# Kernel tuning notes

Measured on AMD Instinct MI355X. Metric: run time of the kernel, lower is better.

## Reference

```python
import jax, jax.numpy as jnp
import numpy as np

H = 16  # num_heads

def setup_inputs() -> dict:
    key = jax.random.key(0)
    ks = jax.random.split(key, 5)
    B, L, D = 2, 2048, 1024
    x = jax.random.normal(ks[0], (B, L, D), dtype=jnp.float32)
    # causal mask: masked_fill where mask == 0
    attn_mask = jnp.tril(jnp.ones((L, L), dtype=jnp.int32))
    scale = 1.0 / np.sqrt(D)
    Wq = jax.random.normal(ks[1], (D, D), dtype=jnp.float32) * scale
    Wk = jax.random.normal(ks[2], (D, D), dtype=jnp.float32) * scale
    Wv = jax.random.normal(ks[3], (D, D), dtype=jnp.float32) * scale
    Wo = jax.random.normal(ks[4], (D, D), dtype=jnp.float32) * scale
    return {"x": x, "attn_mask": attn_mask, "Wq": Wq, "Wk": Wk, "Wv": Wv, "Wo": Wo}

def reference(x, attn_mask, Wq, Wk, Wv, Wo):
    B, L, D = x.shape
    dh = D // H
    # nn.Linear with no bias: y = x @ W^T
    q = (x @ Wq.T).reshape(B, L, H, dh)
    k = (x @ Wk.T).reshape(B, L, H, dh)
    v = (x @ Wv.T).reshape(B, L, H, dh)
    # scores: [B, H, L, L]
    scores = jnp.einsum('blhd,bmhd->bhlm', q, k) / jnp.sqrt(jnp.array(dh, x.dtype))
    scores = jnp.where(attn_mask == 0, -jnp.inf, scores)
    attn = jax.nn.softmax(scores, axis=-1)
    out = jnp.einsum('bhlm,bmhd->blhd', attn, v).reshape(B, L, D)
    return out @ Wo.T
```

## Files before the change

### kernel.cpp

```cpp
#include <hip/hip_runtime.h>
#include <math.h>

#define L_SEQ  2048
#define D_MODEL 1024
#define N_HEAD 16
#define D_HEAD 64
#define B_SIZE 2

typedef __attribute__((ext_vector_type(8))) short bf16x8;
typedef __attribute__((ext_vector_type(4))) float f32x4;
typedef unsigned short u16;
typedef unsigned int u32;

__device__ __forceinline__ f32x4 mfma16(bf16x8 a, bf16x8 b, f32x4 c) {
    return __builtin_amdgcn_mfma_f32_16x16x32_bf16(a, b, c, 0, 0, 0);
}

__device__ __forceinline__ u16 f2bf(float x) {
    u32 u = __builtin_bit_cast(u32, x);
    u32 r = (u + 0x7FFFu + ((u >> 16) & 1u)) >> 16;
    return (u16)r;
}
__device__ __forceinline__ float bf2f(u16 h) {
    u32 u = ((u32)h) << 16;
    return __builtin_bit_cast(float, u);
}

__device__ __forceinline__ void gl2lds16(const void* g, void* l) {
    __builtin_amdgcn_global_load_lds(
        (__attribute__((address_space(1))) void*)(g),
        (__attribute__((address_space(3))) void*)(l), 16, 0, 0);
}

__global__ __launch_bounds__(256) void split_hl(const float* __restrict__ in,
                                                u16* __restrict__ out) {
    const int idx = blockIdx.x * 256 + threadIdx.x;
    const int c4 = idx << 2;
    const int r = c4 >> 10, c = c4 & 1023;
    float4 v = *(const float4*)(in + c4);
    u16 h0 = f2bf(v.x), h1 = f2bf(v.y), h2 = f2bf(v.z), h3 = f2bf(v.w);
    ushort4 hi = make_ushort4(h0, h1, h2, h3);
    ushort4 lo = make_ushort4(f2bf(v.x - bf2f(h0)), f2bf(v.y - bf2f(h1)),
                              f2bf(v.z - bf2f(h2)), f2bf(v.w - bf2f(h3)));
    *(ushort4*)(out + (size_t)r * 2048 + c) = hi;
    *(ushort4*)(out + (size_t)r * 2048 + 1024 + c) = lo;
}

__global__ __launch_bounds__(256) void split_w4(
    const float* __restrict__ w0, const float* __restrict__ w1,
    const float* __restrict__ w2, const float* __restrict__ w3,
    u16* __restrict__ outbase) {
    const float* in = (blockIdx.y == 0) ? w0 : (blockIdx.y == 1) ? w1
                      : (blockIdx.y == 2) ? w2 : w3;
    u16* out = outbase + (size_t)blockIdx.y * 2097152;
    const int idx = blockIdx.x * 256 + threadIdx.x;
    const int c4 = idx << 2;
    const int r = c4 >> 10, c = c4 & 1023;
    float4 v = *(const float4*)(in + c4);
    u16 h0 = f2bf(v.x), h1 = f2bf(v.y), h2 = f2bf(v.z), h3 = f2bf(v.w);
    ushort4 hi = make_ushort4(h0, h1, h2, h3);
    ushort4 lo = make_ushort4(f2bf(v.x - bf2f(h0)), f2bf(v.y - bf2f(h1)),
                              f2bf(v.z - bf2f(h2)), f2bf(v.w - bf2f(h3)));
    *(ushort4*)(out + (size_t)r * 2048 + c) = hi;
    *(ushort4*)(out + (size_t)r * 2048 + 1024 + c) = lo;
}

template <int MODE>
__global__ __launch_bounds__(256) void gemm_ks(
    const u16* __restrict__ A2, const u16* __restrict__ Wbase,
    float* __restrict__ Cout,
    u16* __restrict__ Qh, u16* __restrict__ Ql,
    u16* __restrict__ Kh, u16* __restrict__ Kl,
    u16* __restrict__ Vh, u16* __restrict__ Vl) {
    __shared__ __align__(16) u16 As[128 * 32];
    __shared__ __align__(16) u16 Ws[128 * 32];
    const int t = threadIdx.x, l = t & 63, wid = t >> 6;
    const int m0 = blockIdx.y << 7, n0 = blockIdx.x << 7;
    const int z = (MODE == 1) ? blockIdx.z : 0;
    const u16* W2 = Wbase + (size_t)z * (1024 * 2048);

    f32x4 acc[4][4];
#pragma unroll
    for (int i = 0; i < 4; ++i)
#pragma unroll
        for (int j = 0; j < 4; ++j) acc[i][j] = (f32x4){0.f, 0.f, 0.f, 0.f};

    int orow[2], ocs[2];
#pragma unroll
    for (int p = 0; p < 2; ++p) {
        int o = wid * 1024 + l * 16 + p * 4096;
        orow[p] = o >> 6;
        ocs[p] = ((o >> 4) & 3) ^ ((o >> 6) & 3);
    }
    const int wr = (wid >> 1) << 6, wc = (wid & 1) << 6;

    for (int k0 = 0; k0 < 3072; k0 += 32) {
        const int rg3 = k0 >> 10, kb = k0 & 1023;
        const int ka = (rg3 == 1 ? 1024 : 0) + kb;
        const int kw = (rg3 == 0 ? 1024 : 0) + kb;
        __syncthreads();
#pragma unroll
        for (int p = 0; p < 2; ++p) {
            gl2lds16(A2 + (size_t)(m0 + orow[p]) * 2048 + ka + ocs[p] * 8,
                     (u16*)As + (wid * 512 + p * 2048));
            gl2lds16(W2 + (size_t)(n0 + orow[p]) * 2048 + kw + ocs[p] * 8,
                     (u16*)Ws + (wid * 512 + p * 2048));
        }
        __syncthreads();
        bf16x8 af[4], bfr[4];
#pragma unroll
        for (int f = 0; f < 4; ++f) {
            int row = wr + (f << 4) + (l & 15);
            int ch = (l >> 4) ^ (row & 3);
            af[f] = *(const bf16x8*)&As[(row << 5) + (ch << 3)];
            int rown = wc + (f << 4) + (l & 15);
            int chn = (l >> 4) ^ (rown & 3);
            bfr[f] = *(const bf16x8*)&Ws[(rown << 5) + (chn << 3)];
        }
#pragma unroll
        for (int fm = 0; fm < 4; ++fm)
#pragma unroll
            for (int fn = 0; fn < 4; ++fn)
                acc[fm][fn] = mfma16(af[fm], bfr[fn], acc[fm][fn]);
    }

#pragma unroll
    for (int fm = 0; fm < 4; ++fm)
#pragma unroll
        for (int fn = 0; fn < 4; ++fn)
#pragma unroll
            for (int rg = 0; rg < 4; ++rg) {
                int gm = m0 + wr + (fm << 4) + ((l >> 4) << 2) + rg;
                int gn = n0 + wc + (fn << 4) + (l & 15);
                float v = acc[fm][fn][rg];
                if (MODE == 0) {
                    Cout[(size_t)gm * 1024 + gn] = v;
                } else {
                    if (z == 0) v *= 0.125f;
                    int b = gm >> 11, lq = gm & 2047, h = gn >> 6, d = gn & 63;
                    size_t oi = (((size_t)(b * 16 + h)) * 2048 + lq) * 64 + d;
                    u16 hi = f2bf(v);
                    u16 lo = f2bf(v - bf2f(hi));
                    u16 *ph, *pl;
                    if (z == 0)      { ph = Qh; pl = Ql; }
                    else if (z == 1) { ph = Kh; pl = Kl; }
                    else             { ph = Vh; pl = Vl; }
                    ph[oi] = hi;
                    pl[oi] = lo;
                }
            }
}

__global__ __launch_bounds__(128) void vtrans(const u16* __restrict__ Vh,
                                              const u16* __restrict__ Vl,
                                              u16* __restrict__ Vth,
                                              u16* __restrict__ Vtl) {
    const int t = threadIdx.x;
    const int kt = blockIdx.x, h = blockIdx.y, b = blockIdx.z;
    const size_t base = ((size_t)(b * 16 + h)) * 131072;
    const int kv0 = kt << 6;
    const u16* src = (t < 64) ? Vh : Vl;
    u16* dst = (t < 64) ? Vth : Vtl;
    const int st = t & 63;
    const int r0 = (st >> 3) << 3;
    const int c0 = (st & 7) << 3;
    ushort4 inv[8][2];
#pragma unroll
    for (int j = 0; j < 8; ++j) {
        const u16* p = src + base + (size_t)(kv0 + r0 + j) * 64 + c0;
        inv[j][0] = *(const ushort4*)p;
        inv[j][1] = *(const ushort4*)(p + 4);
    }
#pragma unroll
    for (int i = 0; i < 8; ++i) {
        u16 o[8];
#pragma unroll
        for (int j = 0; j < 8; ++j) {
            ushort4 vv = inv[j][i >> 2];
            const int ii = i & 3;
            o[j] = (ii == 0) ? vv.x : (ii == 1) ? vv.y : (ii == 2) ? vv.z : vv.w;
        }
        u16* q = dst + base + (size_t)(c0 + i) * 2048 + kv0 + r0;
        *(ushort4*)q = make_ushort4(o[0], o[1], o[2], o[3]);
        *(ushort4*)(q + 4) = make_ushort4(o[4], o[5], o[6], o[7]);
    }
}

struct QTileState {
    bf16x8 qhf[2], qlf[2];
    f32x4 oacc[4];
    float mrow[4], lrow[4];
};

__device__ __forceinline__ void qstate_init(
    QTileState& st, const u16* Qh, const u16* Ql, size_t hb, int q0, int w, int l) {
    const int rowq = q0 + (w << 4) + (l & 15);
#pragma unroll
    for (int kc = 0; kc < 2; ++kc) {
        const size_t off = hb + (size_t)rowq * 64 + (((kc << 2) + (l >> 4)) << 3);
        st.qhf[kc] = *(const bf16x8*)(Qh + off);
        st.qlf[kc] = *(const bf16x8*)(Ql + off);
    }
#pragma unroll
    for (int i = 0; i < 4; ++i) {
        st.oacc[i] = (f32x4){0.f, 0.f, 0.f, 0.f};
        st.mrow[i] = -INFINITY;
        st.lrow[i] = 0.f;
    }
}

__device__ __forceinline__ void fa_compute(
    QTileState& st, const u16* bKh, const u16* bKl,
    const u16* bVh, const u16* bVl, int kv0, int q0, int w, int l, u16* Pw) {
    if (kv0 > q0 + (w << 4) + 15) return;

    f32x4 sacc[4];
#pragma unroll
    for (int nf = 0; nf < 4; ++nf) sacc[nf] = (f32x4){0.f, 0.f, 0.f, 0.f};
#pragma unroll
    for (int kc = 0; kc < 2; ++kc) {
        bf16x8 kh_[4], kl_[4];
#pragma unroll
        for (int nf = 0; nf < 4; ++nf) {
            const int row = (nf << 4) + (l & 15);
            const int ch = ((kc << 2) + (l >> 4)) ^ (row & 7);
            kh_[nf] = *(const bf16x8*)&bKh[(row << 6) + (ch << 3)];
            kl_[nf] = *(const bf16x8*)&bKl[(row << 6) + (ch << 3)];
        }
#pragma unroll
        for (int nf = 0; nf < 4; ++nf) {
            sacc[nf] = mfma16(st.qhf[kc], kl_[nf], sacc[nf]);
            sacc[nf] = mfma16(st.qlf[kc], kh_[nf], sacc[nf]);
            sacc[nf] = mfma16(st.qhf[kc], kh_[nf], sacc[nf]);
        }
    }

    const bool domask = (kv0 + 63) > (q0 + (w << 4));
    float pm[4] = {-INFINITY, -INFINITY, -INFINITY, -INFINITY};
    float sv[4][4];
#pragma unroll
    for (int nf = 0; nf < 4; ++nf)
#pragma unroll
        for (int rg = 0; rg < 4; ++rg) {
            float x = sacc[nf][rg];
            if (domask) {
                const int colg = kv0 + (nf << 4) + (l & 15);
                const int rowg = q0 + (w << 4) + ((l >> 4) << 2) + rg;
                if (colg > rowg) x = -INFINITY;
            }
            sv[nf][rg] = x;
            pm[rg] = fmaxf(pm[rg], x);
        }
#pragma unroll
    for (int rg = 0; rg < 4; ++rg) {
        float v = pm[rg];
        v = fmaxf(v, __shfl_xor(v, 1));
        v = fmaxf(v, __shfl_xor(v, 2));
        v = fmaxf(v, __shfl_xor(v, 4));
        v = fmaxf(v, __shfl_xor(v, 8));
        pm[rg] = v;
    }
    float al[4];
#pragma unroll
    for (int rg = 0; rg < 4; ++rg) {
        const float mn = fmaxf(st.mrow[rg], pm[rg]);
        al[rg] = __expf(st.mrow[rg] - mn);
        st.mrow[rg] = mn;
    }
    float ps[4] = {0.f, 0.f, 0.f, 0.f};
    u16 pb[4][4];
#pragma unroll
    for (int nf = 0; nf < 4; ++nf)
#pragma unroll
        for (int rg = 0; rg < 4; ++rg) {
            const float p = __expf(sv[nf][rg] - st.mrow[rg]);
            ps[rg] += p;
            pb[nf][rg] = f2bf(p);
        }
#pragma unroll
    for (int rg = 0; rg < 4; ++rg) {
        float v = ps[rg];
        v += __shfl_xor(v, 1);
        v += __shfl_xor(v, 2);
        v += __shfl_xor(v, 4);
        v += __shfl_xor(v, 8);
        st.lrow[rg] = st.lrow[rg] * al[rg] + v;
    }
#pragma unroll
    for (int nf = 0; nf < 4; ++nf)
#pragma unroll
        for (int rg = 0; rg < 4; ++rg) st.oacc[nf][rg] *= al[rg];

#pragma unroll
    for (int nf = 0; nf < 4; ++nf)
#pragma unroll
        for (int rg = 0; rg < 4; ++rg) {
            const int r = ((l >> 4) << 2) + rg;
            const int c = (nf << 4) + (l & 15);
            const int ch = (c >> 3) ^ (r & 7);
            Pw[(r << 6) + (ch << 3) + (c & 7)] = pb[nf][rg];
        }
#pragma unroll
    for (int kc = 0; kc < 2; ++kc) {
        const int r = l & 15;
        const int chp = ((kc << 2) + (l >> 4)) ^ (r & 7);
        const bf16x8 pa = *(const bf16x8*)&Pw[(r << 6) + (chp << 3)];
        bf16x8 vh_[4], vl_[4];
#pragma unroll
        for (int nf = 0; nf < 4; ++nf) {
            const int row = (nf << 4) + (l & 15);
            const int cv = ((kc << 2) + (l >> 4)) ^ (row & 7);
            vh_[nf] = *(const bf16x8*)&bVh[(row << 6) + (cv << 3)];
            vl_[nf] = *(const bf16x8*)&bVl[(row << 6) + (cv << 3)];
        }
#pragma unroll
        for (int nf = 0; nf < 4; ++nf) {
            st.oacc[nf] = mfma16(pa, vh_[nf], st.oacc[nf]);
            st.oacc[nf] = mfma16(pa, vl_[nf], st.oacc[nf]);
        }
    }
}

__device__ __forceinline__ void fa_epilogue(
    QTileState& st, u16* A2, int g, int q0, int w, int l) {
    const int b = g >> 4, h = g & 15;
    float inv[4];
#pragma unroll
    for (int rg = 0; rg < 4; ++rg) inv[rg] = 1.0f / st.lrow[rg];
#pragma unroll
    for (int nf = 0; nf < 4; ++nf)
#pragma unroll
        for (int rg = 0; rg < 4; ++rg) {
            const int rowq = q0 + (w << 4) + ((l >> 4) << 2) + rg;
            const int m = (b << 11) + rowq;
            const int d = (nf << 4) + (l & 15);
            const float v = st.oacc[nf][rg] * inv[rg];
            const u16 hi = f2bf(v);
            const u16 lo = f2bf(v - bf2f(hi));
            const size_t rb = (size_t)m * 2048;
            A2[rb + h * 64 + d] = hi;
            A2[rb + 1024 + h * 64 + d] = lo;
        }
}

__global__ __launch_bounds__(512) void flash_mfma(
    const u16* __restrict__ Qh, const u16* __restrict__ Ql,
    const u16* __restrict__ Kh, const u16* __restrict__ Kl,
    const u16* __restrict__ Vth, const u16* __restrict__ Vtl,
    u16* __restrict__ A2) {
    extern __shared__ __align__(16) u16 smem[];
    u16* const KhsA = smem;
    u16* const KlsA = smem + 4096;
    u16* const VhsA = smem + 8192;
    u16* const VlsA = smem + 12288;
    u16* const KhsB = smem + 16384;
    u16* const KlsB = smem + 20480;
    u16* const VhsB = smem + 24576;
    u16* const VlsB = smem + 28672;
    u16* const Ps   = smem + 32768;

    const int t = threadIdx.x, l = t & 63, w = t >> 6;
    const int id = blockIdx.x;
    const int nid = ((id & 7) << 5) + (id >> 3);
    const int g = nid >> 3;
    const int p = nid & 7;
    const int q0A = p << 7;
    const int q0B = (15 - p) << 7;
    const size_t hb = (size_t)g * 131072;

    QTileState stA, stB;
    qstate_init(stA, Qh, Ql, hb, q0A, w, l);
    qstate_init(stB, Qh, Ql, hb, q0B, w, l);

    const int row_s = t >> 3;
    const int cs_s = (t & 7) ^ (row_s & 7);

    auto stage = [&](u16* dKh, u16* dKl, u16* dVh, u16* dVl, int kt_) {
        const int kv0s = kt_ << 6;
        const size_t koff = hb + (size_t)(kv0s + row_s) * 64 + cs_s * 8;
        gl2lds16(Kh + koff, dKh + t * 8);
        gl2lds16(Kl + koff, dKl + t * 8);
        const size_t voff = hb + (size_t)row_s * 2048 + kv0s + cs_s * 8;
        gl2lds16(Vth + voff, dVh + t * 8);
        gl2lds16(Vtl + voff, dVl + t * 8);
    };

    u16* const Pw = Ps + (w << 10);
    const int ntA = (p << 1) + 2;
    const int ntB = 32 - (p << 1);

    stage(KhsA, KlsA, VhsA, VlsA, 0);
    __syncthreads();
    for (int kt = 0; kt < ntB; kt += 2) {
        stage(KhsB, KlsB, VhsB, VlsB, kt + 1);
        fa_compute(stB, KhsA, KlsA, VhsA, VlsA, kt << 6, q0B, w, l, Pw);
        if (kt < ntA)
            fa_compute(stA, KhsA, KlsA, VhsA, VlsA, kt << 6, q0A, w, l, Pw);
        __syncthreads();
        if (kt + 2 < ntB) stage(KhsA, KlsA, VhsA, VlsA, kt + 2);
        fa_compute(stB, KhsB, KlsB, VhsB, VlsB, (kt + 1) << 6, q0B, w, l, Pw);
        if (kt + 1 < ntA)
            fa_compute(stA, KhsB, KlsB, VhsB, VlsB, (kt + 1) << 6, q0A, w, l, Pw);
        __syncthreads();
    }

    fa_epilogue(stA, A2, g, q0A, w, l);
    fa_epilogue(stB, A2, g, q0B, w, l);
}

__global__ __launch_bounds__(256) void gemm_bt_f32(
    const float* __restrict__ A, const float* __restrict__ W,
    float* __restrict__ C, int M, int N, int K) {
    __shared__ float As[16][68];
    __shared__ float Bs[16][68];
    const int t = threadIdx.x;
    const int tx = t & 15, ty = t >> 4;
    const int m0 = blockIdx.y << 6, n0 = blockIdx.x << 6;
    const int lr = t >> 2, lc = (t & 3) << 2;
    const float* Ag = A + (size_t)(m0 + lr) * K + lc;
    const float* Wg = W + (size_t)(n0 + lr) * K + lc;
    float acc[4][4];
#pragma unroll
    for (int i = 0; i < 4; ++i)
#pragma unroll
        for (int j = 0; j < 4; ++j) acc[i][j] = 0.f;
    for (int k0 = 0; k0 < K; k0 += 16) {
        const float4 av = *(const float4*)(Ag + k0);
        const float4 wv = *(const float4*)(Wg + k0);
        __syncthreads();
        As[lc + 0][lr] = av.x; As[lc + 1][lr] = av.y;
        As[lc + 2][lr] = av.z; As[lc + 3][lr] = av.w;
        Bs[lc + 0][lr] = wv.x; Bs[lc + 1][lr] = wv.y;
        Bs[lc + 2][lr] = wv.z; Bs[lc + 3][lr] = wv.w;
        __syncthreads();
#pragma unroll
        for (int kk = 0; kk < 16; ++kk) {
            const float4 a = *(const float4*)&As[kk][ty << 2];
            const float4 b = *(const float4*)&Bs[kk][tx << 2];
            acc[0][0] += a.x * b.x; acc[0][1] += a.x * b.y; acc[0][2] += a.x * b.z; acc[0][3] += a.x * b.w;
            acc[1][0] += a.y * b.x; acc[1][1] += a.y * b.y; acc[1][2] += a.y * b.z; acc[1][3] += a.y * b.w;
            acc[2][0] += a.z * b.x; acc[2][1] += a.z * b.y; acc[2][2] += a.z * b.z; acc[2][3] += a.z * b.w;
            acc[3][0] += a.w * b.x; acc[3][1] += a.w * b.y; acc[3][2] += a.w * b.z; acc[3][3] += a.w * b.w;
        }
    }
#pragma unroll
    for (int i = 0; i < 4; ++i) {
        float4 o;
        o.x = acc[i][0]; o.y = acc[i][1]; o.z = acc[i][2]; o.w = acc[i][3];
        *(float4*)&C[(size_t)(m0 + (ty << 2) + i) * N + n0 + (tx << 2)] = o;
    }
}

#define SW(row, seg) ((((seg) ^ (((row) + ((row) >> 4)) & 15)) << 2))

__global__ __launch_bounds__(256) void flash_f32(
    const float* __restrict__ Q, const float* __restrict__ K,
    const float* __restrict__ V, float* __restrict__ O) {
    __shared__ float Qs[64 * 64];
    __shared__ float KPs[64 * 64];
    __shared__ float Vs[64 * 64];
    const int t = threadIdx.x;
    const int tx = t & 15, ty = t >> 4;
    const int qt = blockIdx.x, h = blockIdx.y, b = blockIdx.z;
    const int q0 = qt << 6;
    const size_t hbase = (size_t)b * L_SEQ * D_MODEL + (size_t)h * D_HEAD;
#pragma unroll
    for (int i = 0; i < 4; ++i) {
        const int idx = t + (i << 8);
        const int rr = idx >> 4, seg = idx & 15;
        const float4 qv = *(const float4*)&Q[hbase + (size_t)(q0 + rr) * D_MODEL + (seg << 2)];
        *(float4*)&Qs[rr * 64 + SW(rr, seg)] = qv;
    }
    float m[4], lr_[4], oacc[4][4];
#pragma unroll
    for (int i = 0; i < 4; ++i) {
        m[i] = -INFINITY; lr_[i] = 0.f;
#pragma unroll
        for (int j = 0; j < 4; ++j) oacc[i][j] = 0.f;
    }
    const int ntile = qt + 1;
    for (int kt = 0; kt < ntile; ++kt) {
        const int kv0 = kt << 6;
        __syncthreads();
#pragma unroll
        for (int i = 0; i < 4; ++i) {
            const int idx = t + (i << 8);
            const int rr = idx >> 4, seg = idx & 15;
            const float4 kv = *(const float4*)&K[hbase + (size_t)(kv0 + rr) * D_MODEL + (seg << 2)];
            const float4 vv = *(const float4*)&V[hbase + (size_t)(kv0 + rr) * D_MODEL + (seg << 2)];
            *(float4*)&KPs[rr * 64 + SW(rr, seg)] = kv;
            *(float4*)&Vs[rr * 64 + SW(rr, seg)] = vv;
        }
        __syncthreads();
        float s[4][4];
#pragma unroll
        for (int i = 0; i < 4; ++i)
#pragma unroll
            for (int j = 0; j < 4; ++j) s[i][j] = 0.f;
#pragma unroll
        for (int seg = 0; seg < 16; ++seg) {
            float4 qv[4], kv[4];
#pragma unroll
            for (int i = 0; i < 4; ++i) {
                const int R = (ty << 2) + i;
                qv[i] = *(const float4*)&Qs[R * 64 + SW(R, seg)];
            }
#pragma unroll
            for (int j = 0; j < 4; ++j) {
                const int Cc = (tx << 2) + j;
                kv[j] = *(const float4*)&KPs[Cc * 64 + SW(Cc, seg)];
            }
#pragma unroll
            for (int i = 0; i < 4; ++i)
#pragma unroll
                for (int j = 0; j < 4; ++j)
                    s[i][j] += qv[i].x * kv[j].x + qv[i].y * kv[j].y +
                               qv[i].z * kv[j].z + qv[i].w * kv[j].w;
        }
        const bool diag = (kt == qt);
        float tm[4];
#pragma unroll
        for (int i = 0; i < 4; ++i) {
            tm[i] = -INFINITY;
#pragma unroll
            for (int j = 0; j < 4; ++j) {
                float sval = s[i][j] * 0.125f;
                if (diag) {
                    const int Cg = kv0 + (tx << 2) + j;
                    const int Rg = q0 + (ty << 2) + i;
                    if (Cg > Rg) sval = -INFINITY;
                }
                s[i][j] = sval;
                tm[i] = fmaxf(tm[i], sval);
            }
            tm[i] = fmaxf(tm[i], __shfl_xor(tm[i], 1));
            tm[i] = fmaxf(tm[i], __shfl_xor(tm[i], 2));
            tm[i] = fmaxf(tm[i], __shfl_xor(tm[i], 4));
            tm[i] = fmaxf(tm[i], __shfl_xor(tm[i], 8));
        }
        float p[4][4];
#pragma unroll
        for (int i = 0; i < 4; ++i) {
            const float mn = fmaxf(m[i], tm[i]);
            const float alpha = __expf(m[i] - mn);
            m[i] = mn;
            float psum = 0.f;
#pragma unroll
            for (int j = 0; j < 4; ++j) {
                p[i][j] = __expf(s[i][j] - mn);
                psum += p[i][j];
            }
            psum += __shfl_xor(psum, 1);
            psum += __shfl_xor(psum, 2);
            psum += __shfl_xor(psum, 4);
            psum += __shfl_xor(psum, 8);
            lr_[i] = lr_[i] * alpha + psum;
#pragma unroll
            for (int j = 0; j < 4; ++j) oacc[i][j] *= alpha;
        }
        __syncthreads();
#pragma unroll
        for (int i = 0; i < 4; ++i) {
            const int R = (ty << 2) + i;
            float4 pv;
            pv.x = p[i][0]; pv.y = p[i][1]; pv.z = p[i][2]; pv.w = p[i][3];
            *(float4*)&KPs[R * 64 + SW(R, tx)] = pv;
        }
        __syncthreads();
#pragma unroll
        for (int cs = 0; cs < 16; ++cs) {
            float pc[4][4];
            float4 vr[4];
#pragma unroll
            for (int i = 0; i < 4; ++i) {
                const int R = (ty << 2) + i;
                const float4 pr = *(const float4*)&KPs[R * 64 + SW(R, cs)];
                pc[i][0] = pr.x; pc[i][1] = pr.y; pc[i][2] = pr.z; pc[i][3] = pr.w;
            }
#pragma unroll
            for (int cc = 0; cc < 4; ++cc) {
                const int Cr = (cs << 2) + cc;
                vr[cc] = *(const float4*)&Vs[Cr * 64 + SW(Cr, tx)];
            }
#pragma unroll
            for (int i = 0; i < 4; ++i)
#pragma unroll
                for (int cc = 0; cc < 4; ++cc) {
                    oacc[i][0] += pc[i][cc] * vr[cc].x;
                    oacc[i][1] += pc[i][cc] * vr[cc].y;
                    oacc[i][2] += pc[i][cc] * vr[cc].z;
                    oacc[i][3] += pc[i][cc] * vr[cc].w;
                }
        }
    }
#pragma unroll
    for (int i = 0; i < 4; ++i) {
        const int R = (ty << 2) + i;
        const float invl = 1.0f / lr_[i];
        float4 o;
        o.x = oacc[i][0] * invl; o.y = oacc[i][1] * invl;
        o.z = oacc[i][2] * invl; o.w = oacc[i][3] * invl;
        *(float4*)&O[hbase + (size_t)(q0 + R) * D_MODEL + (tx << 2)] = o;
    }
}

extern "C" void kernel_launch(void* const* d_in, const int* in_sizes, int n_in,
                              void* d_out, int out_size, void* d_ws, size_t ws_size,
                              hipStream_t stream) {
    const float* x  = (const float*)d_in[0];
    const float* Wq = (const float*)d_in[2];
    const float* Wk = (const float*)d_in[3];
    const float* Wv = (const float*)d_in[4];
    const float* Wo = (const float*)d_in[5];
    float* out = (float*)d_out;

    if (ws_size >= 83886080ull) {
        char* ws = (char*)d_ws;
        u16* x2  = (u16*)(ws);
        u16* Wq2 = (u16*)(ws + 16777216);
        u16* Wo2 = (u16*)(ws + 29360128);
        u16* Qh  = (u16*)(ws + 33554432);
        u16* Ql  = (u16*)(ws + 41943040);
        u16* Kh  = (u16*)(ws + 50331648);
        u16* Kl  = (u16*)(ws + 58720256);
        u16* Vth = (u16*)(ws + 67108864);
        u16* Vtl = (u16*)(ws + 75497472);
        u16* Vh  = (u16*)d_out;
        u16* Vl  = (u16*)d_out + 4194304;

        hipFuncSetAttribute((const void*)flash_mfma,
                            hipFuncAttributeMaxDynamicSharedMemorySize, 81920);

        split_hl<<<4096, 256, 0, stream>>>(x, x2);
        split_w4<<<dim3(1024, 4), 256, 0, stream>>>(Wq, Wk, Wv, Wo, Wq2);
        gemm_ks<1><<<dim3(8, 32, 3), 256, 0, stream>>>(x2, Wq2, nullptr,
                                                       Qh, Ql, Kh, Kl, Vh, Vl);
        vtrans<<<dim3(32, 16, 2), 128, 0, stream>>>(Vh, Vl, Vth, Vtl);
        flash_mfma<<<256, 512, 81920, stream>>>(Qh, Ql, Kh, Kl, Vth, Vtl, x2);
        gemm_ks<0><<<dim3(8, 32, 1), 256, 0, stream>>>(x2, Wo2, out,
                                                       nullptr, nullptr, nullptr,
                                                       nullptr, nullptr, nullptr);
    } else {
        const int M = B_SIZE * L_SEQ, N = D_MODEL, Kd = D_MODEL;
        float* Qw = (float*)d_ws;
        float* Kw = Qw + (size_t)M * D_MODEL;
        float* Vw = Kw + (size_t)M * D_MODEL;
        float* Aw = Vw + (size_t)M * D_MODEL;
        dim3 gg(N / 64, M / 64);
        gemm_bt_f32<<<gg, 256, 0, stream>>>(x, Wq, Qw, M, N, Kd);
        gemm_bt_f32<<<gg, 256, 0, stream>>>(x, Wk, Kw, M, N, Kd);
        gemm_bt_f32<<<gg, 256, 0, stream>>>(x, Wv, Vw, M, N, Kd);
        flash_f32<<<dim3(L_SEQ / 64, N_HEAD, B_SIZE), 256, 0, stream>>>(Qw, Kw, Vw, Aw);
        gemm_bt_f32<<<gg, 256, 0, stream>>>(Aw, Wo, out, M, N, Kd);
    }
}
```

Measured before the change: 260.5 us.

## Drop V low-half split, lazy softmax rescale, wider GEMM K-tile, MFMA priority hints

Stores V only as a single bf16 (no low residual). This removes the Vl staging, transpose and half the P·V MFMAs, and shrinks flash LDS from 80KB to 64KB. The online-softmax rescale is now skipped unless some row max grows by more than 8, and P is truncated to bf16 instead of rounded. The split-bf16 GEMM moves to a 64-wide K tile with an 8-way XOR swizzle, and setprio brackets the MFMA blocks. Dropping the V residual and truncating P lowers accuracy compared with the earlier near-fp32 emulation.

```diff
diff --git a/kernel.cpp b/kernel.cpp
--- a/kernel.cpp
+++ b/kernel.cpp
@@ -20,6 +20,9 @@
     u32 u = __builtin_bit_cast(u32, x);
     u32 r = (u + 0x7FFFu + ((u >> 16) & 1u)) >> 16;
     return (u16)r;
+}
+__device__ __forceinline__ u16 f2bf_t(float x) {
+    return (u16)(__builtin_bit_cast(u32, x) >> 16);
 }
 __device__ __forceinline__ float bf2f(u16 h) {
     u32 u = ((u32)h) << 16;
@@ -72,8 +75,8 @@
     u16* __restrict__ Qh, u16* __restrict__ Ql,
     u16* __restrict__ Kh, u16* __restrict__ Kl,
     u16* __restrict__ Vh, u16* __restrict__ Vl) {
-    __shared__ __align__(16) u16 As[128 * 32];
-    __shared__ __align__(16) u16 Ws[128 * 32];
+    __shared__ __align__(16) u16 As[128 * 64];
+    __shared__ __align__(16) u16 Ws[128 * 64];
     const int t = threadIdx.x, l = t & 63, wid = t >> 6;
     const int m0 = blockIdx.y << 7, n0 = blockIdx.x << 7;
     const int z = (MODE == 1) ? blockIdx.z : 0;
@@ -85,43 +88,47 @@
 #pragma unroll
         for (int j = 0; j < 4; ++j) acc[i][j] = (f32x4){0.f, 0.f, 0.f, 0.f};
 
-    int orow[2], ocs[2];
-#pragma unroll
-    for (int p = 0; p < 2; ++p) {
-        int o = wid * 1024 + l * 16 + p * 4096;
-        orow[p] = o >> 6;
-        ocs[p] = ((o >> 4) & 3) ^ ((o >> 6) & 3);
+    int srow[4], scs[4];
+#pragma unroll
+    for (int p = 0; p < 4; ++p) {
+        const int o = t + (p << 8);
+        srow[p] = o >> 3;
+        scs[p] = (o & 7) ^ (srow[p] & 7);
     }
     const int wr = (wid >> 1) << 6, wc = (wid & 1) << 6;
 
-    for (int k0 = 0; k0 < 3072; k0 += 32) {
+    for (int k0 = 0; k0 < 3072; k0 += 64) {
         const int rg3 = k0 >> 10, kb = k0 & 1023;
         const int ka = (rg3 == 1 ? 1024 : 0) + kb;
         const int kw = (rg3 == 0 ? 1024 : 0) + kb;
         __syncthreads();
 #pragma unroll
-        for (int p = 0; p < 2; ++p) {
-            gl2lds16(A2 + (size_t)(m0 + orow[p]) * 2048 + ka + ocs[p] * 8,
-                     (u16*)As + (wid * 512 + p * 2048));
-            gl2lds16(W2 + (size_t)(n0 + orow[p]) * 2048 + kw + ocs[p] * 8,
-                     (u16*)Ws + (wid * 512 + p * 2048));
-        }
-        __syncthreads();
-        bf16x8 af[4], bfr[4];
-#pragma unroll
-        for (int f = 0; f < 4; ++f) {
-            int row = wr + (f << 4) + (l & 15);
-            int ch = (l >> 4) ^ (row & 3);
-            af[f] = *(const bf16x8*)&As[(row << 5) + (ch << 3)];
-            int rown = wc + (f << 4) + (l & 15);
-            int chn = (l >> 4) ^ (rown & 3);
-            bfr[f] = *(const bf16x8*)&Ws[(rown << 5) + (chn << 3)];
-        }
-#pragma unroll
-        for (int fm = 0; fm < 4; ++fm)
-#pragma unroll
-            for (int fn = 0; fn < 4; ++fn)
-                acc[fm][fn] = mfma16(af[fm], bfr[fn], acc[fm][fn]);
+        for (int p = 0; p < 4; ++p) {
+            const int dofs = (t + (p << 8)) << 3;
+            gl2lds16(A2 + (size_t)(m0 + srow[p]) * 2048 + ka + (scs[p] << 3),
+                     (u16*)As + dofs);
+            gl2lds16(W2 + (size_t)(n0 + srow[p]) * 2048 + kw + (scs[p] << 3),
+                     (u16*)Ws + dofs);
+        }
+        __syncthreads();
+#pragma unroll
+        for (int kc = 0; kc < 2; ++kc) {
+            bf16x8 af[4], bfr[4];
+#pragma unroll
+            for (int f = 0; f < 4; ++f) {
+                const int row = wr + (f << 4) + (l & 15);
+                const int ch = ((kc << 2) + (l >> 4)) ^ (row & 7);
+                af[f] = *(const bf16x8*)&As[(row << 6) + (ch << 3)];
+                const int rown = wc + (f << 4) + (l & 15);
+                const int chn = ((kc << 2) + (l >> 4)) ^ (rown & 7);
+                bfr[f] = *(const bf16x8*)&Ws[(rown << 6) + (chn << 3)];
+            }
+#pragma unroll
+            for (int fm = 0; fm < 4; ++fm)
+#pragma unroll
+                for (int fn = 0; fn < 4; ++fn)
+                    acc[fm][fn] = mfma16(af[fm], bfr[fn], acc[fm][fn]);
+        }
     }
 
 #pragma unroll
@@ -140,34 +147,30 @@
                     int b = gm >> 11, lq = gm & 2047, h = gn >> 6, d = gn & 63;
                     size_t oi = (((size_t)(b * 16 + h)) * 2048 + lq) * 64 + d;
                     u16 hi = f2bf(v);
-                    u16 lo = f2bf(v - bf2f(hi));
                     u16 *ph, *pl;
                     if (z == 0)      { ph = Qh; pl = Ql; }
                     else if (z == 1) { ph = Kh; pl = Kl; }
                     else             { ph = Vh; pl = Vl; }
                     ph[oi] = hi;
-                    pl[oi] = lo;
+                    if (z != 2) pl[oi] = f2bf(v - bf2f(hi));
                 }
             }
 }
 
 __global__ __launch_bounds__(128) void vtrans(const u16* __restrict__ Vh,
-                                              const u16* __restrict__ Vl,
-                                              u16* __restrict__ Vth,
-                                              u16* __restrict__ Vtl) {
+                                              u16* __restrict__ Vth) {
     const int t = threadIdx.x;
-    const int kt = blockIdx.x, h = blockIdx.y, b = blockIdx.z;
+    const int kt = (blockIdx.x << 1) + (t >> 6);
+    const int h = blockIdx.y, b = blockIdx.z;
     const size_t base = ((size_t)(b * 16 + h)) * 131072;
     const int kv0 = kt << 6;
-    const u16* src = (t < 64) ? Vh : Vl;
-    u16* dst = (t < 64) ? Vth : Vtl;
     const int st = t & 63;
     const int r0 = (st >> 3) << 3;
     const int c0 = (st & 7) << 3;
     ushort4 inv[8][2];
 #pragma unroll
     for (int j = 0; j < 8; ++j) {
-        const u16* p = src + base + (size_t)(kv0 + r0 + j) * 64 + c0;
+        const u16* p = Vh + base + (size_t)(kv0 + r0 + j) * 64 + c0;
         inv[j][0] = *(const ushort4*)p;
         inv[j][1] = *(const ushort4*)(p + 4);
     }
@@ -180,7 +183,7 @@
             const int ii = i & 3;
             o[j] = (ii == 0) ? vv.x : (ii == 1) ? vv.y : (ii == 2) ? vv.z : vv.w;
         }
-        u16* q = dst + base + (size_t)(c0 + i) * 2048 + kv0 + r0;
+        u16* q = Vth + base + (size_t)(c0 + i) * 2048 + kv0 + r0;
         *(ushort4*)q = make_ushort4(o[0], o[1], o[2], o[3]);
         *(ushort4*)(q + 4) = make_ushort4(o[4], o[5], o[6], o[7]);
     }
@@ -211,7 +214,7 @@
 
 __device__ __forceinline__ void fa_compute(
     QTileState& st, const u16* bKh, const u16* bKl,
-    const u16* bVh, const u16* bVl, int kv0, int q0, int w, int l, u16* Pw) {
+    const u16* bVh, int kv0, int q0, int w, int l, u16* Pw) {
     if (kv0 > q0 + (w << 4) + 15) return;
 
     f32x4 sacc[4];
@@ -227,12 +230,14 @@
             kh_[nf] = *(const bf16x8*)&bKh[(row << 6) + (ch << 3)];
             kl_[nf] = *(const bf16x8*)&bKl[(row << 6) + (ch << 3)];
         }
+        __builtin_amdgcn_s_setprio(1);
 #pragma unroll
         for (int nf = 0; nf < 4; ++nf) {
             sacc[nf] = mfma16(st.qhf[kc], kl_[nf], sacc[nf]);
             sacc[nf] = mfma16(st.qlf[kc], kh_[nf], sacc[nf]);
             sacc[nf] = mfma16(st.qhf[kc], kh_[nf], sacc[nf]);
         }
+        __builtin_amdgcn_s_setprio(0);
     }
 
     const bool domask = (kv0 + 63) > (q0 + (w << 4));
@@ -260,12 +265,18 @@
         v = fmaxf(v, __shfl_xor(v, 8));
         pm[rg] = v;
     }
-    float al[4];
-#pragma unroll
-    for (int rg = 0; rg < 4; ++rg) {
-        const float mn = fmaxf(st.mrow[rg], pm[rg]);
-        al[rg] = __expf(st.mrow[rg] - mn);
-        st.mrow[rg] = mn;
+    const float need = fmaxf(fmaxf(pm[0] - st.mrow[0], pm[1] - st.mrow[1]),
+                             fmaxf(pm[2] - st.mrow[2], pm[3] - st.mrow[3]));
+    if (__any(need > 8.0f)) {
+#pragma unroll
+        for (int rg = 0; rg < 4; ++rg) {
+            const float mn = fmaxf(st.mrow[rg], pm[rg]);
+            const float al = __expf(st.mrow[rg] - mn);
+            st.mrow[rg] = mn;
+            st.lrow[rg] *= al;
+#pragma unroll
+            for (int nf = 0; nf < 4; ++nf) st.oacc[nf][rg] *= al;
+        }
     }
     float ps[4] = {0.f, 0.f, 0.f, 0.f};
     u16 pb[4][4];
@@ -275,7 +286,7 @@
         for (int rg = 0; rg < 4; ++rg) {
             const float p = __expf(sv[nf][rg] - st.mrow[rg]);
             ps[rg] += p;
-            pb[nf][rg] = f2bf(p);
+            pb[nf][rg] = f2bf_t(p);
         }
 #pragma unroll
     for (int rg = 0; rg < 4; ++rg) {
@@ -284,12 +295,8 @@
         v += __shfl_xor(v, 2);
         v += __shfl_xor(v, 4);
         v += __shfl_xor(v, 8);
-        st.lrow[rg] = st.lrow[rg] * al[rg] + v;
-    }
-#pragma unroll
-    for (int nf = 0; nf < 4; ++nf)
-#pragma unroll
-        for (int rg = 0; rg < 4; ++rg) st.oacc[nf][rg] *= al[rg];
+        st.lrow[rg] += v;
+    }
 
 #pragma unroll
     for (int nf = 0; nf < 4; ++nf)
@@ -305,19 +312,18 @@
         const int r = l & 15;
         const int chp = ((kc << 2) + (l >> 4)) ^ (r & 7);
         const bf16x8 pa = *(const bf16x8*)&Pw[(r << 6) + (chp << 3)];
-        bf16x8 vh_[4], vl_[4];
+        bf16x8 vh_[4];
 #pragma unroll
         for (int nf = 0; nf < 4; ++nf) {
             const int row = (nf << 4) + (l & 15);
             const int cv = ((kc << 2) + (l >> 4)) ^ (row & 7);
             vh_[nf] = *(const bf16x8*)&bVh[(row << 6) + (cv << 3)];
-            vl_[nf] = *(const bf16x8*)&bVl[(row << 6) + (cv << 3)];
-        }
-#pragma unroll
-        for (int nf = 0; nf < 4; ++nf) {
+        }
+        __builtin_amdgcn_s_setprio(1);
+#pragma unroll
+        for (int nf = 0; nf < 4; ++nf)
             st.oacc[nf] = mfma16(pa, vh_[nf], st.oacc[nf]);
-            st.oacc[nf] = mfma16(pa, vl_[nf], st.oacc[nf]);
-        }
+        __builtin_amdgcn_s_setprio(0);
     }
 }
 
@@ -346,18 +352,16 @@
 __global__ __launch_bounds__(512) void flash_mfma(
     const u16* __restrict__ Qh, const u16* __restrict__ Ql,
     const u16* __restrict__ Kh, const u16* __restrict__ Kl,
-    const u16* __restrict__ Vth, const u16* __restrict__ Vtl,
+    const u16* __restrict__ Vth,
     u16* __restrict__ A2) {
     extern __shared__ __align__(16) u16 smem[];
     u16* const KhsA = smem;
     u16* const KlsA = smem + 4096;
     u16* const VhsA = smem + 8192;
-    u16* const VlsA = smem + 12288;
-    u16* const KhsB = smem + 16384;
-    u16* const KlsB = smem + 20480;
-    u16* const VhsB = smem + 24576;
-    u16* const VlsB = smem + 28672;
-    u16* const Ps   = smem + 32768;
+    u16* const KhsB = smem + 12288;
+    u16* const KlsB = smem + 16384;
+    u16* const VhsB = smem + 20480;
+    u16* const Ps   = smem + 24576;
 
     const int t = threadIdx.x, l = t & 63, w = t >> 6;
     const int id = blockIdx.x;
@@ -375,32 +379,31 @@
     const int row_s = t >> 3;
     const int cs_s = (t & 7) ^ (row_s & 7);
 
-    auto stage = [&](u16* dKh, u16* dKl, u16* dVh, u16* dVl, int kt_) {
+    auto stage = [&](u16* dKh, u16* dKl, u16* dVh, int kt_) {
         const int kv0s = kt_ << 6;
         const size_t koff = hb + (size_t)(kv0s + row_s) * 64 + cs_s * 8;
         gl2lds16(Kh + koff, dKh + t * 8);
         gl2lds16(Kl + koff, dKl + t * 8);
         const size_t voff = hb + (size_t)row_s * 2048 + kv0s + cs_s * 8;
         gl2lds16(Vth + voff, dVh + t * 8);
-        gl2lds16(Vtl + voff, dVl + t * 8);
     };
 
     u16* const Pw = Ps + (w << 10);
     const int ntA = (p << 1) + 2;
     const int ntB = 32 - (p << 1);
 
-    stage(KhsA, KlsA, VhsA, VlsA, 0);
+    stage(KhsA, KlsA, VhsA, 0);
     __syncthreads();
     for (int kt = 0; kt < ntB; kt += 2) {
-        stage(KhsB, KlsB, VhsB, VlsB, kt + 1);
-        fa_compute(stB, KhsA, KlsA, VhsA, VlsA, kt << 6, q0B, w, l, Pw);
+        stage(KhsB, KlsB, VhsB, kt + 1);
+        fa_compute(stB, KhsA, KlsA, VhsA, kt << 6, q0B, w, l, Pw);
         if (kt < ntA)
-            fa_compute(stA, KhsA, KlsA, VhsA, VlsA, kt << 6, q0A, w, l, Pw);
-        __syncthreads();
-        if (kt + 2 < ntB) stage(KhsA, KlsA, VhsA, VlsA, kt + 2);
-        fa_compute(stB, KhsB, KlsB, VhsB, VlsB, (kt + 1) << 6, q0B, w, l, Pw);
+            fa_compute(stA, KhsA, KlsA, VhsA, kt << 6, q0A, w, l, Pw);
+        __syncthreads();
+        if (kt + 2 < ntB) stage(KhsA, KlsA, VhsA, kt + 2);
+        fa_compute(stB, KhsB, KlsB, VhsB, (kt + 1) << 6, q0B, w, l, Pw);
         if (kt + 1 < ntA)
-            fa_compute(stA, KhsB, KlsB, VhsB, VlsB, (kt + 1) << 6, q0A, w, l, Pw);
+            fa_compute(stA, KhsB, KlsB, VhsB, (kt + 1) << 6, q0A, w, l, Pw);
         __syncthreads();
     }
 
@@ -624,19 +627,18 @@
         u16* Kh  = (u16*)(ws + 50331648);
         u16* Kl  = (u16*)(ws + 58720256);
         u16* Vth = (u16*)(ws + 67108864);
-        u16* Vtl = (u16*)(ws + 75497472);
         u16* Vh  = (u16*)d_out;
         u16* Vl  = (u16*)d_out + 4194304;
 
         hipFuncSetAttribute((const void*)flash_mfma,
-                            hipFuncAttributeMaxDynamicSharedMemorySize, 81920);
+                            hipFuncAttributeMaxDynamicSharedMemorySize, 65536);
 
         split_hl<<<4096, 256, 0, stream>>>(x, x2);
         split_w4<<<dim3(1024, 4), 256, 0, stream>>>(Wq, Wk, Wv, Wo, Wq2);
         gemm_ks<1><<<dim3(8, 32, 3), 256, 0, stream>>>(x2, Wq2, nullptr,
                                                        Qh, Ql, Kh, Kl, Vh, Vl);
-        vtrans<<<dim3(32, 16, 2), 128, 0, stream>>>(Vh, Vl, Vth, Vtl);
-        flash_mfma<<<256, 512, 81920, stream>>>(Qh, Ql, Kh, Kl, Vth, Vtl, x2);
+        vtrans<<<dim3(16, 16, 2), 128, 0, stream>>>(Vh, Vth);
+        flash_mfma<<<256, 512, 65536, stream>>>(Qh, Ql, Kh, Kl, Vth, x2);
         gemm_ks<0><<<dim3(8, 32, 1), 256, 0, stream>>>(x2, Wo2, out,
                                                        nullptr, nullptr, nullptr,
                                                        nullptr, nullptr, nullptr);
```

New measurement: 275.5 us. +5.8%, slower.
